# Optimization experiments

Hardware: AMD Instinct MI355X
Metric: run time of the kernel (lower is better)

Reference implementation:

```python
import jax, jax.numpy as jnp
import numpy as np

B, S, F_IN, E, H = 8, 1024, 512, 512, 8
C = E // H  # chunk size per head


def setup_inputs() -> dict:
    key = jax.random.key(0)
    ks = jax.random.split(key, 20)
    sF = 1.0 / np.sqrt(F_IN)
    sE = 1.0 / np.sqrt(E)
    d = {
        'x_real': jax.random.normal(ks[0], (B, S, F_IN), jnp.float32),
        'x_imag': jax.random.normal(ks[1], (B, S, F_IN), jnp.float32),
    }
    names = ['q', 'k', 'v']
    for i, n in enumerate(names):
        d[f'w{n}_r'] = jax.random.normal(ks[2 + 4 * i], (E, F_IN), jnp.float32) * sF
        d[f'w{n}_i'] = jax.random.normal(ks[3 + 4 * i], (E, F_IN), jnp.float32) * sF
        d[f'b{n}_r'] = jax.random.normal(ks[4 + 4 * i], (E,), jnp.float32) * sF
        d[f'b{n}_i'] = jax.random.normal(ks[5 + 4 * i], (E,), jnp.float32) * sF
    d['wo_r'] = jax.random.normal(ks[14], (F_IN, E), jnp.float32) * sE
    d['wo_i'] = jax.random.normal(ks[15], (F_IN, E), jnp.float32) * sE
    d['bo_r'] = jax.random.normal(ks[16], (F_IN,), jnp.float32) * sE
    d['bo_i'] = jax.random.normal(ks[17], (F_IN,), jnp.float32) * sE
    return d


def _cplx(r, i):
    return jax.lax.complex(r, i)


def _heads(y):
    # (B, S, E) -> (B, H, S, C); matches split(dim=2)+stack+transpose(0,1)
    return y.reshape(B, S, H, C).transpose(0, 2, 1, 3)


def reference(x_real, x_imag,
              wq_r, wq_i, bq_r, bq_i,
              wk_r, wk_i, bk_r, bk_i,
              wv_r, wv_i, bv_r, bv_i,
              wo_r, wo_i, bo_r, bo_i):
    x = _cplx(x_real, x_imag)
    wq, wk, wv = _cplx(wq_r, wq_i), _cplx(wk_r, wk_i), _cplx(wv_r, wv_i)
    bq, bk, bv = _cplx(bq_r, bq_i), _cplx(bk_r, bk_i), _cplx(bv_r, bv_i)
    wo, bo = _cplx(wo_r, wo_i), _cplx(bo_r, bo_i)

    q = _heads(jnp.einsum('bsf,ef->bse', x, wq) + bq)  # (B,H,S,C) complex
    k = _heads(jnp.einsum('bsf,ef->bse', x, wk) + bk)
    v = _heads(jnp.einsum('bsf,ef->bse', x, wv) + bv)

    divisor = jnp.sqrt(jnp.float32(2 * C))
    # Hermitian inner product: q @ conj(k)^T -> (B,H,S,S)
    sim = jnp.einsum('bhsc,bhtc->bhst', q, jnp.conj(k)) / divisor
    attn = jax.nn.softmax(jnp.abs(sim), axis=3).astype(jnp.complex64)
    # second Hermitian bmm: attn @ conj(v)
    av = jnp.einsum('bhst,bhtc->bhsc', attn, jnp.conj(v))
    concat = av.transpose(0, 2, 1, 3).reshape(B, S, E)
    out = jnp.einsum('bse,fe->bsf', concat, wo) + bo
    return out, attn
```

## Files before the change

kernel.cpp:

```cpp
#include <hip/hip_runtime.h>


namespace {
constexpr int Bn = 8, Sn = 1024, Fn = 512, En = 512, Hn = 8, Cn = 64;
constexpr int Mn = Bn * Sn;
constexpr int Qszi = Bn * Hn * Sn * Cn;
constexpr size_t Qsz = (size_t)Qszi;
constexpr int XLIM = Bn * Sn * Fn;
constexpr int WLIM = En * Fn;
constexpr size_t OUT1 = (size_t)Bn * Sn * Fn;
constexpr size_t ATT1 = (size_t)Bn * Hn * Sn * Sn;
constexpr float RDIV = 0.08838834764831845f;
}

typedef __attribute__((ext_vector_type(8))) short short8v;
typedef __attribute__((ext_vector_type(4))) float f32x4;

__device__ __forceinline__ size_t cmin(size_t i, size_t lim) { return i < lim ? i : lim; }

__device__ __forceinline__ float bf2f(unsigned short u) {
    union { unsigned int u32; float f; } c; c.u32 = (unsigned int)u << 16; return c.f;
}
__device__ __forceinline__ unsigned short f2bf(float f) {
    union { float f; unsigned int u; } c; c.f = f;
    unsigned int r = (c.u + 0x7FFFu + ((c.u >> 16) & 1u)) >> 16;
    return (unsigned short)r;
}
__device__ __forceinline__ unsigned int packbf(float lo, float hi) {
    return (unsigned int)f2bf(lo) | ((unsigned int)f2bf(hi) << 16);
}
__device__ __forceinline__ short8v neg8(short8v v) {
    union { short8v s; unsigned int u[4]; } c; c.s = v;
    #pragma unroll
    for (int j = 0; j < 4; ++j) c.u[j] ^= 0x80008000u;
    return c.s;
}

__device__ __forceinline__ float4 ld4(const float* p) { return *(const float4*)p; }
__device__ __forceinline__ float4 ld4(const unsigned short* p) {
    ushort4 v = *(const ushort4*)p;
    return make_float4(bf2f(v.x), bf2f(v.y), bf2f(v.z), bf2f(v.w));
}

template<bool CONJB>
__device__ __forceinline__ void mfma_body(
    const short (*As_r)[40], const short (*As_i)[40],
    const short (*Bs_r)[40], const short (*Bs_i)[40],
    int wr, int wn, int lrow, int lk,
    f32x4 accr[4][2], f32x4 acci[4][2])
{
    short8v a_r[4], a_i[4], a_x[4];
    #pragma unroll
    for (int fm = 0; fm < 4; ++fm) {
        a_r[fm] = *(const short8v*)&As_r[wr*64 + fm*16 + lrow][lk];
        a_i[fm] = *(const short8v*)&As_i[wr*64 + fm*16 + lrow][lk];
        a_x[fm] = neg8(CONJB ? a_r[fm] : a_i[fm]);
    }
    short8v b_r[2], b_i[2];
    #pragma unroll
    for (int fn = 0; fn < 2; ++fn) {
        b_r[fn] = *(const short8v*)&Bs_r[wn*32 + fn*16 + lrow][lk];
        b_i[fn] = *(const short8v*)&Bs_i[wn*32 + fn*16 + lrow][lk];
    }
    #pragma unroll
    for (int fm = 0; fm < 4; ++fm)
        #pragma unroll
        for (int fn = 0; fn < 2; ++fn) {
            accr[fm][fn] = __builtin_amdgcn_mfma_f32_16x16x32_bf16(
                a_r[fm], b_r[fn], accr[fm][fn], 0, 0, 0);
            accr[fm][fn] = __builtin_amdgcn_mfma_f32_16x16x32_bf16(
                CONJB ? a_i[fm] : a_x[fm], b_i[fn], accr[fm][fn], 0, 0, 0);
            acci[fm][fn] = __builtin_amdgcn_mfma_f32_16x16x32_bf16(
                CONJB ? a_x[fm] : a_r[fm], b_i[fn], acci[fm][fn], 0, 0, 0);
            acci[fm][fn] = __builtin_amdgcn_mfma_f32_16x16x32_bf16(
                a_i[fm], b_r[fn], acci[fm][fn], 0, 0, 0);
        }
}

template<bool CONJB>
__device__ __forceinline__ void cgemm_mfma(
    const float* __restrict__ Ar, const float* __restrict__ Ai, int arow0, int lda,
    const float* __restrict__ Br, const float* __restrict__ Bi, int brow0, int ldb,
    int K, f32x4 accr[4][2], f32x4 acci[4][2])
{
    __shared__ short As_r[128][40], As_i[128][40];
    __shared__ short Bs_r[64][40],  Bs_i[64][40];
    const int tid = threadIdx.x;
    const int sar = tid >> 1, sac = (tid & 1) * 16;
    const int sbr = tid >> 2, sbc = (tid & 3) * 8;
    const int wid = tid >> 6, lane = tid & 63;
    const int wr = wid >> 1, wn = wid & 1;
    const int lrow = lane & 15, lk = (lane >> 4) * 8;

    for (int k0 = 0; k0 < K; k0 += 32) {
        const float* pAr = Ar + (size_t)(arow0 + sar) * lda + k0 + sac;
        const float* pAi = Ai + (size_t)(arow0 + sar) * lda + k0 + sac;
        float4 va_r[4], va_i[4];
        #pragma unroll
        for (int q = 0; q < 4; ++q) { va_r[q] = ld4(pAr + 4*q); va_i[q] = ld4(pAi + 4*q); }
        const float* pBr = Br + (size_t)(brow0 + sbr) * ldb + k0 + sbc;
        const float* pBi = Bi + (size_t)(brow0 + sbr) * ldb + k0 + sbc;
        float4 vb_r[2], vb_i[2];
        #pragma unroll
        for (int q = 0; q < 2; ++q) { vb_r[q] = ld4(pBr + 4*q); vb_i[q] = ld4(pBi + 4*q); }

        __syncthreads();
        #pragma unroll
        for (int q = 0; q < 4; ++q) {
            *(uint2*)&As_r[sar][sac + 4*q] =
                make_uint2(packbf(va_r[q].x, va_r[q].y), packbf(va_r[q].z, va_r[q].w));
            *(uint2*)&As_i[sar][sac + 4*q] =
                make_uint2(packbf(va_i[q].x, va_i[q].y), packbf(va_i[q].z, va_i[q].w));
        }
        #pragma unroll
        for (int q = 0; q < 2; ++q) {
            *(uint2*)&Bs_r[sbr][sbc + 4*q] =
                make_uint2(packbf(vb_r[q].x, vb_r[q].y), packbf(vb_r[q].z, vb_r[q].w));
            *(uint2*)&Bs_i[sbr][sbc + 4*q] =
                make_uint2(packbf(vb_i[q].x, vb_i[q].y), packbf(vb_i[q].z, vb_i[q].w));
        }
        __syncthreads();
        mfma_body<CONJB>(As_r, As_i, Bs_r, Bs_i, wr, wn, lrow, lk, accr, acci);
    }
}

template<bool CONJB>
__device__ __forceinline__ void cgemm_mfma_bf16(
    const unsigned short* __restrict__ Ar, const unsigned short* __restrict__ Ai,
    int arow0, int lda,
    const unsigned short* __restrict__ Br, const unsigned short* __restrict__ Bi,
    int brow0, int ldb,
    int K, f32x4 accr[4][2], f32x4 acci[4][2])
{
    __shared__ short As_r[128][40], As_i[128][40];
    __shared__ short Bs_r[64][40],  Bs_i[64][40];
    const int tid = threadIdx.x;
    const int sar = tid >> 1, sac = (tid & 1) * 16;
    const int sbr = tid >> 2, sbc = (tid & 3) * 8;
    const int wid = tid >> 6, lane = tid & 63;
    const int wr = wid >> 1, wn = wid & 1;
    const int lrow = lane & 15, lk = (lane >> 4) * 8;

    for (int k0 = 0; k0 < K; k0 += 32) {
        const unsigned short* pAr = Ar + (size_t)(arow0 + sar) * lda + k0 + sac;
        const unsigned short* pAi = Ai + (size_t)(arow0 + sar) * lda + k0 + sac;
        short8v va_r0 = *(const short8v*)pAr;
        short8v va_r1 = *(const short8v*)(pAr + 8);
        short8v va_i0 = *(const short8v*)pAi;
        short8v va_i1 = *(const short8v*)(pAi + 8);
        const unsigned short* pBr = Br + (size_t)(brow0 + sbr) * ldb + k0 + sbc;
        const unsigned short* pBi = Bi + (size_t)(brow0 + sbr) * ldb + k0 + sbc;
        short8v vb_r = *(const short8v*)pBr;
        short8v vb_i = *(const short8v*)pBi;

        __syncthreads();
        *(short8v*)&As_r[sar][sac]     = va_r0;
        *(short8v*)&As_r[sar][sac + 8] = va_r1;
        *(short8v*)&As_i[sar][sac]     = va_i0;
        *(short8v*)&As_i[sar][sac + 8] = va_i1;
        *(short8v*)&Bs_r[sbr][sbc] = vb_r;
        *(short8v*)&Bs_i[sbr][sbc] = vb_i;
        __syncthreads();
        mfma_body<CONJB>(As_r, As_i, Bs_r, Bs_i, wr, wn, lrow, lk, accr, acci);
    }
}

__global__ void diag_k(float* __restrict__ out, float v) { out[0] = v; }

__global__ __launch_bounds__(256) void qkv_proj_k(
    const float* __restrict__ xr, const float* __restrict__ xi,
    const float* __restrict__ wqr, const float* __restrict__ wqi,
    const float* __restrict__ bqr, const float* __restrict__ bqi,
    const float* __restrict__ wkr, const float* __restrict__ wki,
    const float* __restrict__ bkr, const float* __restrict__ bki,
    const float* __restrict__ wvr, const float* __restrict__ wvi,
    const float* __restrict__ bvr, const float* __restrict__ bvi,
    unsigned short* __restrict__ ws)
{
    const int which = blockIdx.z;
    const float* wr_ = which == 0 ? wqr : which == 1 ? wkr : wvr;
    const float* wi_ = which == 0 ? wqi : which == 1 ? wki : wvi;
    const float* br_ = which == 0 ? bqr : which == 1 ? bkr : bvr;
    const float* bi_ = which == 0 ? bqi : which == 1 ? bki : bvi;
    unsigned short* outr = ws + (size_t)which * 2 * Qsz;
    unsigned short* outi = outr + Qsz;

    const int m0 = blockIdx.x * 128, n0 = blockIdx.y * 64;
    f32x4 accr[4][2], acci[4][2];
    const f32x4 z4 = {0.f, 0.f, 0.f, 0.f};
    #pragma unroll
    for (int fm = 0; fm < 4; ++fm)
        #pragma unroll
        for (int fn = 0; fn < 2; ++fn) { accr[fm][fn] = z4; acci[fm][fn] = z4; }

    cgemm_mfma<false>(xr, xi, m0, Fn, wr_, wi_, n0, Fn, Fn, accr, acci);

    const int lane = threadIdx.x & 63, wid = threadIdx.x >> 6;
    const int wr2 = wid >> 1, wn2 = wid & 1;
    #pragma unroll
    for (int fm = 0; fm < 4; ++fm)
        #pragma unroll
        for (int fn = 0; fn < 2; ++fn) {
            const int e = n0 + wn2*32 + fn*16 + (lane & 15);
            const int h = e >> 6, c = e & (Cn - 1);
            const float brv = br_[e], biv = bi_[e];
            #pragma unroll
            for (int r = 0; r < 4; ++r) {
                const int m = m0 + wr2*64 + fm*16 + (lane >> 4)*4 + r;
                const int b = m >> 10, s = m & (Sn - 1);
                const size_t idx = (((size_t)(b * Hn + h)) * Sn + s) * Cn + c;
                outr[idx] = f2bf(accr[fm][fn][r] + brv);
                outi[idx] = f2bf(acci[fm][fn][r] + biv);
            }
        }
}

template<int ST>
__global__ __launch_bounds__(256) void score_k(
    const unsigned short* __restrict__ qkv, float* __restrict__ attn)
{
    const int bh = blockIdx.z;
    const int r0 = blockIdx.x * 128, t0 = blockIdx.y * 64;
    const int row0 = bh * Sn;

    f32x4 accr[4][2], acci[4][2];
    const f32x4 z4 = {0.f, 0.f, 0.f, 0.f};
    #pragma unroll
    for (int fm = 0; fm < 4; ++fm)
        #pragma unroll
        for (int fn = 0; fn < 2; ++fn) { accr[fm][fn] = z4; acci[fm][fn] = z4; }

    cgemm_mfma_bf16<true>(qkv, qkv + Qsz, row0 + r0, Cn,
                          qkv + 2 * Qsz, qkv + 3 * Qsz, row0 + t0, Cn,
                          Cn, accr, acci);

    const size_t ATTF = ATT1 * ST;
    const int lane = threadIdx.x & 63, wid = threadIdx.x >> 6;
    const int wr2 = wid >> 1, wn2 = wid & 1;
    #pragma unroll
    for (int fm = 0; fm < 4; ++fm)
        #pragma unroll
        for (int fn = 0; fn < 2; ++fn) {
            const int t = t0 + wn2*32 + fn*16 + (lane & 15);
            #pragma unroll
            for (int r = 0; r < 4; ++r) {
                const int srow = r0 + wr2*64 + fm*16 + (lane >> 4)*4 + r;
                const size_t row = (size_t)bh * Sn + srow;
                const float re = accr[fm][fn][r], im = acci[fm][fn][r];
                const float mag = sqrtf(fmaf(re, re, im*im)) * RDIV;
                const size_t idx = cmin((row * Sn + t) * (size_t)ST, ATTF - ST);
                if (ST == 2) *(float2*)&attn[idx] = make_float2(mag, 0.f);
                else         attn[idx] = mag;
            }
        }
}

template<int ST>
__global__ __launch_bounds__(256) void softmax_k(float* __restrict__ attn)
{
    const int bh = blockIdx.y;
    const int wid = threadIdx.x >> 6, lane = threadIdx.x & 63;
    const int row = blockIdx.x * 4 + wid;
    const size_t rbase = ((size_t)bh * Sn + row) * Sn;
    const size_t ATTF = ATT1 * ST;

    float v[16];
    float mx = -1e30f;
    #pragma unroll
    for (int j = 0; j < 16; ++j) {
        v[j] = attn[cmin((rbase + lane + 64*j) * (size_t)ST, ATTF - ST)];
        mx = fmaxf(mx, v[j]);
    }
    #pragma unroll
    for (int m = 32; m >= 1; m >>= 1) mx = fmaxf(mx, __shfl_xor(mx, m));
    float sum = 0.f;
    #pragma unroll
    for (int j = 0; j < 16; ++j) { v[j] = __expf(v[j] - mx); sum += v[j]; }
    #pragma unroll
    for (int m = 32; m >= 1; m >>= 1) sum += __shfl_xor(sum, m);
    const float inv = 1.f / sum;
    #pragma unroll
    for (int j = 0; j < 16; ++j)
        attn[cmin((rbase + lane + 64*j) * (size_t)ST, ATTF - ST)] = v[j] * inv;
}

template<int ST>
__global__ __launch_bounds__(256) void av_k(
    const unsigned short* __restrict__ qkv, const float* __restrict__ attn,
    float* __restrict__ av)
{
    const int bh = blockIdx.y;
    const int r0 = blockIdx.x * 128;
    const size_t voff = (size_t)bh * Sn * Cn;
    const unsigned short* vr = qkv + 4 * Qsz + voff;
    const unsigned short* vi = qkv + 5 * Qsz + voff;
    const size_t abase = ((size_t)bh * Sn + r0) * Sn;

    __shared__ short Ps[128][40];
    __shared__ short Vtr[64][40], Vti[64][40];

    const int tid = threadIdx.x;
    const int spr = tid >> 1, spt = (tid & 1) * 16;
    const int svt = tid & 31, svc = (tid >> 5) * 8;
    const int wid = tid >> 6, lane = tid & 63;
    const int wr = wid >> 1, wn = wid & 1;
    const int lrow = lane & 15, lk = (lane >> 4) * 8;

    f32x4 accr[4][2], acci[4][2];
    const f32x4 z4 = {0.f, 0.f, 0.f, 0.f};
    #pragma unroll
    for (int fm = 0; fm < 4; ++fm)
        #pragma unroll
        for (int fn = 0; fn < 2; ++fn) { accr[fm][fn] = z4; acci[fm][fn] = z4; }

    for (int t0 = 0; t0 < Sn; t0 += 32) {
        float pv[16];
        if (ST == 2) {
            const float4* ap4 = (const float4*)((const float2*)attn +
                                 (abase + (size_t)spr * Sn + t0 + spt));
            #pragma unroll
            for (int q = 0; q < 8; ++q) { float4 v4 = ap4[q]; pv[2*q] = v4.x; pv[2*q+1] = v4.z; }
        } else {
            const float* ap = attn + abase + (size_t)spr * Sn + t0 + spt;
            #pragma unroll
            for (int q = 0; q < 4; ++q) {
                float4 v4 = *(const float4*)(ap + 4*q);
                pv[4*q] = v4.x; pv[4*q+1] = v4.y; pv[4*q+2] = v4.z; pv[4*q+3] = v4.w;
            }
        }
        short8v vvr = *(const short8v*)(vr + (size_t)(t0 + svt) * Cn + svc);
        short8v vvi = *(const short8v*)(vi + (size_t)(t0 + svt) * Cn + svc);

        __syncthreads();
        #pragma unroll
        for (int q = 0; q < 4; ++q)
            *(unsigned int*)&Ps[spr][spt + 4*q] =
                (unsigned int)f2bf(pv[4*q])     | ((unsigned int)f2bf(pv[4*q+1]) << 16),
            *(unsigned int*)&Ps[spr][spt + 4*q + 2] =
                (unsigned int)f2bf(pv[4*q+2])   | ((unsigned int)f2bf(pv[4*q+3]) << 16);
        #pragma unroll
        for (int j = 0; j < 8; ++j) {
            Vtr[svc + j][svt] = vvr[j];
            Vti[svc + j][svt] = vvi[j];
        }
        __syncthreads();

        short8v pA[4];
        #pragma unroll
        for (int fm = 0; fm < 4; ++fm)
            pA[fm] = *(const short8v*)&Ps[wr*64 + fm*16 + lrow][lk];
        short8v bR[2], bI[2];
        #pragma unroll
        for (int fn = 0; fn < 2; ++fn) {
            bR[fn] = *(const short8v*)&Vtr[wn*32 + fn*16 + lrow][lk];
            bI[fn] = *(const short8v*)&Vti[wn*32 + fn*16 + lrow][lk];
        }
        #pragma unroll
        for (int fm = 0; fm < 4; ++fm)
            #pragma unroll
            for (int fn = 0; fn < 2; ++fn) {
                accr[fm][fn] = __builtin_amdgcn_mfma_f32_16x16x32_bf16(
                    pA[fm], bR[fn], accr[fm][fn], 0, 0, 0);
                acci[fm][fn] = __builtin_amdgcn_mfma_f32_16x16x32_bf16(
                    pA[fm], bI[fn], acci[fm][fn], 0, 0, 0);
            }
    }

    const int b = bh >> 3, h = bh & 7;
    #pragma unroll
    for (int fm = 0; fm < 4; ++fm)
        #pragma unroll
        for (int fn = 0; fn < 2; ++fn) {
            const int c = wn*32 + fn*16 + (lane & 15);
            #pragma unroll
            for (int r = 0; r < 4; ++r) {
                const int srow = r0 + wr*64 + fm*16 + (lane >> 4)*4 + r;
                const size_t base = ((size_t)(b * Sn + srow)) * En + h * Cn + c;
                av[base]       =  accr[fm][fn][r];
                av[Qsz + base] = -acci[fm][fn][r];
            }
        }
}

template<int ST>
__global__ __launch_bounds__(256) void out_proj_k(
    const float* __restrict__ avr, const float* __restrict__ avi,
    const float* __restrict__ wor, const float* __restrict__ woi,
    const float* __restrict__ bor, const float* __restrict__ boi,
    float* __restrict__ out)
{
    const int m0 = blockIdx.x * 128, n0 = blockIdx.y * 64;
    f32x4 accr[4][2], acci[4][2];
    const f32x4 z4 = {0.f, 0.f, 0.f, 0.f};
    #pragma unroll
    for (int fm = 0; fm < 4; ++fm)
        #pragma unroll
        for (int fn = 0; fn < 2; ++fn) { accr[fm][fn] = z4; acci[fm][fn] = z4; }

    cgemm_mfma<false>(avr, avi, m0, En, wor, woi, n0, En, En, accr, acci);

    const int lane = threadIdx.x & 63, wid = threadIdx.x >> 6;
    const int wr2 = wid >> 1, wn2 = wid & 1;
    #pragma unroll
    for (int fm = 0; fm < 4; ++fm)
        #pragma unroll
        for (int fn = 0; fn < 2; ++fn) {
            const int f = n0 + wn2*32 + fn*16 + (lane & 15);
            const float brv = bor[f], biv = boi[f];
            #pragma unroll
            for (int r = 0; r < 4; ++r) {
                const int m = m0 + wr2*64 + fm*16 + (lane >> 4)*4 + r;
                const size_t idx = ((size_t)m * Fn + f) * (size_t)ST;
                if (ST == 2)
                    *(float2*)&out[idx] = make_float2(accr[fm][fn][r] + brv, acci[fm][fn][r] + biv);
                else
                    out[idx] = accr[fm][fn][r] + brv;
            }
        }
}

template<int ST>
static void launch_all(const float* xr, const float* xi,
                       const float* wqr, const float* wqi, const float* bqr, const float* bqi,
                       const float* wkr, const float* wki, const float* bkr, const float* bki,
                       const float* wvr, const float* wvi, const float* bvr, const float* bvi,
                       const float* wor, const float* woi, const float* bor, const float* boi,
                       unsigned short* qkv, float* av, float* out, hipStream_t stream)
{
    float* attn = out + OUT1 * ST;
    qkv_proj_k<<<dim3(Mn/128, En/64, 3), 256, 0, stream>>>(
        xr, xi, wqr, wqi, bqr, bqi, wkr, wki, bkr, bki, wvr, wvi, bvr, bvi, qkv);
    score_k<ST><<<dim3(Sn/128, Sn/64, Bn*Hn), 256, 0, stream>>>(qkv, attn);
    softmax_k<ST><<<dim3(Sn/4, Bn*Hn), 256, 0, stream>>>(attn);
    av_k<ST><<<dim3(Sn/128, Bn*Hn), 256, 0, stream>>>(qkv, attn, av);
    out_proj_k<ST><<<dim3(Mn/128, Fn/64), 256, 0, stream>>>(
        av, av + Qsz, wor, woi, bor, boi, out);
}

extern "C" void kernel_launch(void* const* d_in, const int* in_sizes, int n_in,
                              void* d_out, int out_size, void* d_ws, size_t ws_size,
                              hipStream_t stream)
{
    bool sizes_ok = (n_in == 18);
    if (sizes_ok) {
        sizes_ok = in_sizes[0] == XLIM && in_sizes[1] == XLIM;
        for (int g = 0; g < 3 && sizes_ok; ++g) {
            sizes_ok = in_sizes[2 + 4*g] == WLIM && in_sizes[3 + 4*g] == WLIM &&
                       in_sizes[4 + 4*g] == En  && in_sizes[5 + 4*g] == En;
        }
        sizes_ok = sizes_ok && in_sizes[14] == WLIM && in_sizes[15] == WLIM &&
                   in_sizes[16] == Fn && in_sizes[17] == Fn;
    }
    const size_t ws_needed = 6 * Qsz * sizeof(unsigned short);
    const bool ws_ok = (d_ws != nullptr) && (ws_size >= ws_needed);

    const long long fullF = 2LL * (long long)(OUT1 + ATT1);
    const long long realF = (long long)(OUT1 + ATT1);
    const int st = ((long long)out_size == fullF) ? 2
                 : ((long long)out_size == realF) ? 1 : 0;

    if (!sizes_ok || !ws_ok || st == 0) {
        float diag = !sizes_ok ? 3.0e9f
                   : !ws_ok    ? (float)(double)ws_size
                               : (float)out_size;
        diag_k<<<1, 1, 0, stream>>>((float*)d_out, diag);
        return;
    }

    const float* xr  = (const float*)d_in[0];
    const float* xi  = (const float*)d_in[1];
    const float* wqr = (const float*)d_in[2];
    const float* wqi = (const float*)d_in[3];
    const float* bqr = (const float*)d_in[4];
    const float* bqi = (const float*)d_in[5];
    const float* wkr = (const float*)d_in[6];
    const float* wki = (const float*)d_in[7];
    const float* bkr = (const float*)d_in[8];
    const float* bki = (const float*)d_in[9];
    const float* wvr = (const float*)d_in[10];
    const float* wvi = (const float*)d_in[11];
    const float* bvr = (const float*)d_in[12];
    const float* bvi = (const float*)d_in[13];
    const float* wor = (const float*)d_in[14];
    const float* woi = (const float*)d_in[15];
    const float* bor = (const float*)d_in[16];
    const float* boi = (const float*)d_in[17];

    unsigned short* qkv = (unsigned short*)d_ws;
    float* av = (float*)d_ws;
    float* out = (float*)d_out;

    if (st == 2)
        launch_all<2>(xr, xi, wqr, wqi, bqr, bqi, wkr, wki, bkr, bki,
                      wvr, wvi, bvr, bvi, wor, woi, bor, boi, qkv, av, out, stream);
    else
        launch_all<1>(xr, xi, wqr, wqi, bqr, bqi, wkr, wki, bkr, bki,
                      wvr, wvi, bvr, bvi, wor, woi, bor, boi, qkv, av, out, stream);
}
```

Before: 394.5 us.

## Fuse score, softmax and attn@V into one two-pass attention kernel

Replaces the separate score, softmax and attn@V kernels with one kernel per (batch-head, 128-row) tile. A first pass recomputes the Hermitian QK scores to build softmax row sums. A second pass recomputes them, writes normalized probabilities once, and multiplies them by V from LDS. Since |sim| is non-negative and small, the row max is skipped. This removes the read-modify-write round trips of the large attention matrix through global memory, at the cost of computing QK twice. The attention-value output is now stored as bf16 in a separate workspace region, which halves the out-projection A-operand traffic and requires a larger workspace.

```diff
diff --git a/kernel.cpp b/kernel.cpp
--- a/kernel.cpp
+++ b/kernel.cpp
@@ -16,8 +16,6 @@
 typedef __attribute__((ext_vector_type(8))) short short8v;
 typedef __attribute__((ext_vector_type(4))) float f32x4;
 
-__device__ __forceinline__ size_t cmin(size_t i, size_t lim) { return i < lim ? i : lim; }
-
 __device__ __forceinline__ float bf2f(unsigned short u) {
     union { unsigned int u32; float f; } c; c.u32 = (unsigned int)u << 16; return c.f;
 }
@@ -35,12 +33,7 @@
     for (int j = 0; j < 4; ++j) c.u[j] ^= 0x80008000u;
     return c.s;
 }
-
 __device__ __forceinline__ float4 ld4(const float* p) { return *(const float4*)p; }
-__device__ __forceinline__ float4 ld4(const unsigned short* p) {
-    ushort4 v = *(const ushort4*)p;
-    return make_float4(bf2f(v.x), bf2f(v.y), bf2f(v.z), bf2f(v.w));
-}
 
 template<bool CONJB>
 __device__ __forceinline__ void mfma_body(
@@ -125,11 +118,10 @@
 }
 
 template<bool CONJB>
-__device__ __forceinline__ void cgemm_mfma_bf16(
+__device__ __forceinline__ void cgemm_mfma_abf16(
     const unsigned short* __restrict__ Ar, const unsigned short* __restrict__ Ai,
     int arow0, int lda,
-    const unsigned short* __restrict__ Br, const unsigned short* __restrict__ Bi,
-    int brow0, int ldb,
+    const float* __restrict__ Br, const float* __restrict__ Bi, int brow0, int ldb,
     int K, f32x4 accr[4][2], f32x4 acci[4][2])
 {
     __shared__ short As_r[128][40], As_i[128][40];
@@ -148,18 +140,24 @@
         short8v va_r1 = *(const short8v*)(pAr + 8);
         short8v va_i0 = *(const short8v*)pAi;
         short8v va_i1 = *(const short8v*)(pAi + 8);
-        const unsigned short* pBr = Br + (size_t)(brow0 + sbr) * ldb + k0 + sbc;
-        const unsigned short* pBi = Bi + (size_t)(brow0 + sbr) * ldb + k0 + sbc;
-        short8v vb_r = *(const short8v*)pBr;
-        short8v vb_i = *(const short8v*)pBi;
+        const float* pBr = Br + (size_t)(brow0 + sbr) * ldb + k0 + sbc;
+        const float* pBi = Bi + (size_t)(brow0 + sbr) * ldb + k0 + sbc;
+        float4 vb_r[2], vb_i[2];
+        #pragma unroll
+        for (int q = 0; q < 2; ++q) { vb_r[q] = ld4(pBr + 4*q); vb_i[q] = ld4(pBi + 4*q); }
 
         __syncthreads();
         *(short8v*)&As_r[sar][sac]     = va_r0;
         *(short8v*)&As_r[sar][sac + 8] = va_r1;
         *(short8v*)&As_i[sar][sac]     = va_i0;
         *(short8v*)&As_i[sar][sac + 8] = va_i1;
-        *(short8v*)&Bs_r[sbr][sbc] = vb_r;
-        *(short8v*)&Bs_i[sbr][sbc] = vb_i;
+        #pragma unroll
+        for (int q = 0; q < 2; ++q) {
+            *(uint2*)&Bs_r[sbr][sbc + 4*q] =
+                make_uint2(packbf(vb_r[q].x, vb_r[q].y), packbf(vb_r[q].z, vb_r[q].w));
+            *(uint2*)&Bs_i[sbr][sbc + 4*q] =
+                make_uint2(packbf(vb_i[q].x, vb_i[q].y), packbf(vb_i[q].z, vb_i[q].w));
+        }
         __syncthreads();
         mfma_body<CONJB>(As_r, As_i, Bs_r, Bs_i, wr, wn, lrow, lk, accr, acci);
     }
@@ -216,175 +214,237 @@
 }
 
 template<int ST>
-__global__ __launch_bounds__(256) void score_k(
-    const unsigned short* __restrict__ qkv, float* __restrict__ attn)
-{
-    const int bh = blockIdx.z;
-    const int r0 = blockIdx.x * 128, t0 = blockIdx.y * 64;
-    const int row0 = bh * Sn;
-
-    f32x4 accr[4][2], acci[4][2];
-    const f32x4 z4 = {0.f, 0.f, 0.f, 0.f};
-    #pragma unroll
-    for (int fm = 0; fm < 4; ++fm)
-        #pragma unroll
-        for (int fn = 0; fn < 2; ++fn) { accr[fm][fn] = z4; acci[fm][fn] = z4; }
-
-    cgemm_mfma_bf16<true>(qkv, qkv + Qsz, row0 + r0, Cn,
-                          qkv + 2 * Qsz, qkv + 3 * Qsz, row0 + t0, Cn,
-                          Cn, accr, acci);
-
-    const size_t ATTF = ATT1 * ST;
-    const int lane = threadIdx.x & 63, wid = threadIdx.x >> 6;
-    const int wr2 = wid >> 1, wn2 = wid & 1;
-    #pragma unroll
-    for (int fm = 0; fm < 4; ++fm)
-        #pragma unroll
-        for (int fn = 0; fn < 2; ++fn) {
-            const int t = t0 + wn2*32 + fn*16 + (lane & 15);
-            #pragma unroll
-            for (int r = 0; r < 4; ++r) {
-                const int srow = r0 + wr2*64 + fm*16 + (lane >> 4)*4 + r;
-                const size_t row = (size_t)bh * Sn + srow;
-                const float re = accr[fm][fn][r], im = acci[fm][fn][r];
-                const float mag = sqrtf(fmaf(re, re, im*im)) * RDIV;
-                const size_t idx = cmin((row * Sn + t) * (size_t)ST, ATTF - ST);
-                if (ST == 2) *(float2*)&attn[idx] = make_float2(mag, 0.f);
-                else         attn[idx] = mag;
-            }
-        }
-}
-
-template<int ST>
-__global__ __launch_bounds__(256) void softmax_k(float* __restrict__ attn)
-{
-    const int bh = blockIdx.y;
-    const int wid = threadIdx.x >> 6, lane = threadIdx.x & 63;
-    const int row = blockIdx.x * 4 + wid;
-    const size_t rbase = ((size_t)bh * Sn + row) * Sn;
-    const size_t ATTF = ATT1 * ST;
-
-    float v[16];
-    float mx = -1e30f;
-    #pragma unroll
-    for (int j = 0; j < 16; ++j) {
-        v[j] = attn[cmin((rbase + lane + 64*j) * (size_t)ST, ATTF - ST)];
-        mx = fmaxf(mx, v[j]);
-    }
-    #pragma unroll
-    for (int m = 32; m >= 1; m >>= 1) mx = fmaxf(mx, __shfl_xor(mx, m));
-    float sum = 0.f;
-    #pragma unroll
-    for (int j = 0; j < 16; ++j) { v[j] = __expf(v[j] - mx); sum += v[j]; }
-    #pragma unroll
-    for (int m = 32; m >= 1; m >>= 1) sum += __shfl_xor(sum, m);
-    const float inv = 1.f / sum;
-    #pragma unroll
-    for (int j = 0; j < 16; ++j)
-        attn[cmin((rbase + lane + 64*j) * (size_t)ST, ATTF - ST)] = v[j] * inv;
-}
-
-template<int ST>
-__global__ __launch_bounds__(256) void av_k(
-    const unsigned short* __restrict__ qkv, const float* __restrict__ attn,
-    float* __restrict__ av)
+__global__ __launch_bounds__(256) void attn_fused_k(
+    const unsigned short* __restrict__ qkv, float* __restrict__ attn,
+    unsigned short* __restrict__ avb)
 {
     const int bh = blockIdx.y;
     const int r0 = blockIdx.x * 128;
-    const size_t voff = (size_t)bh * Sn * Cn;
-    const unsigned short* vr = qkv + 4 * Qsz + voff;
-    const unsigned short* vi = qkv + 5 * Qsz + voff;
-    const size_t abase = ((size_t)bh * Sn + r0) * Sn;
-
-    __shared__ short Ps[128][40];
-    __shared__ short Vtr[64][40], Vti[64][40];
+    const size_t poff = (size_t)bh * Sn * Cn;
+    const unsigned short* qr = qkv + poff;
+    const unsigned short* qi = qkv + Qsz + poff;
+    const unsigned short* kr = qkv + 2 * Qsz + poff;
+    const unsigned short* ki = qkv + 3 * Qsz + poff;
+    const unsigned short* vr = qkv + 4 * Qsz + poff;
+    const unsigned short* vi = qkv + 5 * Qsz + poff;
+
+    __shared__ short Qr[128][68], Qi[128][68];
+    __shared__ short KP[2][64][68];
+    __shared__ short Vtr[64][68], Vti[64][68];
+    short (*Ps)[68] = (short(*)[68])KP;
 
     const int tid = threadIdx.x;
-    const int spr = tid >> 1, spt = (tid & 1) * 16;
-    const int svt = tid & 31, svc = (tid >> 5) * 8;
-    const int wid = tid >> 6, lane = tid & 63;
+    const int lane = tid & 63, wid = tid >> 6;
+    const int lrow = lane & 15, g = lane >> 4, lk = g * 8;
+    const int srow0 = 32 * wid;
     const int wr = wid >> 1, wn = wid & 1;
-    const int lrow = lane & 15, lk = (lane >> 4) * 8;
-
-    f32x4 accr[4][2], acci[4][2];
+
+    {
+        const int row = tid >> 1, seg = (tid & 1) * 32;
+        const unsigned short* pr = qr + (size_t)(r0 + row) * Cn + seg;
+        const unsigned short* pi = qi + (size_t)(r0 + row) * Cn + seg;
+        #pragma unroll
+        for (int q = 0; q < 4; ++q) {
+            *(short8v*)&Qr[row][seg + 8*q] = *(const short8v*)(pr + 8*q);
+            *(short8v*)&Qi[row][seg + 8*q] = *(const short8v*)(pi + 8*q);
+        }
+    }
+    const int kst_row = tid >> 2, kst_seg = (tid & 3) * 16;
+    const int vst_t = tid & 63, vst_c = (tid >> 6) * 16;
+
+    float ssum[2][4] = {};
+    __syncthreads();
+
+    for (int t0 = 0; t0 < Sn; t0 += 64) {
+        short8v k_r0 = *(const short8v*)(kr + (size_t)(t0 + kst_row) * Cn + kst_seg);
+        short8v k_r1 = *(const short8v*)(kr + (size_t)(t0 + kst_row) * Cn + kst_seg + 8);
+        short8v k_i0 = *(const short8v*)(ki + (size_t)(t0 + kst_row) * Cn + kst_seg);
+        short8v k_i1 = *(const short8v*)(ki + (size_t)(t0 + kst_row) * Cn + kst_seg + 8);
+        __syncthreads();
+        *(short8v*)&KP[0][kst_row][kst_seg]     = k_r0;
+        *(short8v*)&KP[0][kst_row][kst_seg + 8] = k_r1;
+        *(short8v*)&KP[1][kst_row][kst_seg]     = k_i0;
+        *(short8v*)&KP[1][kst_row][kst_seg + 8] = k_i1;
+        __syncthreads();
+
+        f32x4 cr[2][4], ci[2][4];
+        const f32x4 z4 = {0.f, 0.f, 0.f, 0.f};
+        #pragma unroll
+        for (int fm = 0; fm < 2; ++fm)
+            #pragma unroll
+            for (int fn = 0; fn < 4; ++fn) { cr[fm][fn] = z4; ci[fm][fn] = z4; }
+        #pragma unroll
+        for (int kh = 0; kh < 2; ++kh) {
+            const int kof = kh*32 + lk;
+            short8v br_[4], bi_[4];
+            #pragma unroll
+            for (int fn = 0; fn < 4; ++fn) {
+                br_[fn] = *(const short8v*)&KP[0][fn*16 + lrow][kof];
+                bi_[fn] = *(const short8v*)&KP[1][fn*16 + lrow][kof];
+            }
+            #pragma unroll
+            for (int fm = 0; fm < 2; ++fm) {
+                short8v ar = *(const short8v*)&Qr[srow0 + fm*16 + lrow][kof];
+                short8v ai = *(const short8v*)&Qi[srow0 + fm*16 + lrow][kof];
+                short8v ax = neg8(ar);
+                #pragma unroll
+                for (int fn = 0; fn < 4; ++fn) {
+                    cr[fm][fn] = __builtin_amdgcn_mfma_f32_16x16x32_bf16(ar, br_[fn], cr[fm][fn], 0,0,0);
+                    cr[fm][fn] = __builtin_amdgcn_mfma_f32_16x16x32_bf16(ai, bi_[fn], cr[fm][fn], 0,0,0);
+                    ci[fm][fn] = __builtin_amdgcn_mfma_f32_16x16x32_bf16(ai, br_[fn], ci[fm][fn], 0,0,0);
+                    ci[fm][fn] = __builtin_amdgcn_mfma_f32_16x16x32_bf16(ax, bi_[fn], ci[fm][fn], 0,0,0);
+                }
+            }
+        }
+        #pragma unroll
+        for (int fm = 0; fm < 2; ++fm)
+            #pragma unroll
+            for (int rr = 0; rr < 4; ++rr) {
+                float acc = 0.f;
+                #pragma unroll
+                for (int fn = 0; fn < 4; ++fn) {
+                    const float re = cr[fm][fn][rr], im = ci[fm][fn][rr];
+                    acc += __expf(sqrtf(fmaf(re, re, im*im)) * RDIV);
+                }
+                ssum[fm][rr] += acc;
+            }
+    }
+    float inv[2][4];
+    #pragma unroll
+    for (int fm = 0; fm < 2; ++fm)
+        #pragma unroll
+        for (int rr = 0; rr < 4; ++rr) {
+            float s = ssum[fm][rr];
+            s += __shfl_xor(s, 1); s += __shfl_xor(s, 2);
+            s += __shfl_xor(s, 4); s += __shfl_xor(s, 8);
+            inv[fm][rr] = 1.f / s;
+        }
+
+    f32x4 pvr[4][2], pvi[4][2];
     const f32x4 z4 = {0.f, 0.f, 0.f, 0.f};
     #pragma unroll
     for (int fm = 0; fm < 4; ++fm)
         #pragma unroll
-        for (int fn = 0; fn < 2; ++fn) { accr[fm][fn] = z4; acci[fm][fn] = z4; }
-
-    for (int t0 = 0; t0 < Sn; t0 += 32) {
-        float pv[16];
-        if (ST == 2) {
-            const float4* ap4 = (const float4*)((const float2*)attn +
-                                 (abase + (size_t)spr * Sn + t0 + spt));
-            #pragma unroll
-            for (int q = 0; q < 8; ++q) { float4 v4 = ap4[q]; pv[2*q] = v4.x; pv[2*q+1] = v4.z; }
-        } else {
-            const float* ap = attn + abase + (size_t)spr * Sn + t0 + spt;
-            #pragma unroll
-            for (int q = 0; q < 4; ++q) {
-                float4 v4 = *(const float4*)(ap + 4*q);
-                pv[4*q] = v4.x; pv[4*q+1] = v4.y; pv[4*q+2] = v4.z; pv[4*q+3] = v4.w;
-            }
-        }
-        short8v vvr = *(const short8v*)(vr + (size_t)(t0 + svt) * Cn + svc);
-        short8v vvi = *(const short8v*)(vi + (size_t)(t0 + svt) * Cn + svc);
-
-        __syncthreads();
-        #pragma unroll
-        for (int q = 0; q < 4; ++q)
-            *(unsigned int*)&Ps[spr][spt + 4*q] =
-                (unsigned int)f2bf(pv[4*q])     | ((unsigned int)f2bf(pv[4*q+1]) << 16),
-            *(unsigned int*)&Ps[spr][spt + 4*q + 2] =
-                (unsigned int)f2bf(pv[4*q+2])   | ((unsigned int)f2bf(pv[4*q+3]) << 16);
+        for (int fn = 0; fn < 2; ++fn) { pvr[fm][fn] = z4; pvi[fm][fn] = z4; }
+
+    for (int t0 = 0; t0 < Sn; t0 += 64) {
+        short8v k_r0 = *(const short8v*)(kr + (size_t)(t0 + kst_row) * Cn + kst_seg);
+        short8v k_r1 = *(const short8v*)(kr + (size_t)(t0 + kst_row) * Cn + kst_seg + 8);
+        short8v k_i0 = *(const short8v*)(ki + (size_t)(t0 + kst_row) * Cn + kst_seg);
+        short8v k_i1 = *(const short8v*)(ki + (size_t)(t0 + kst_row) * Cn + kst_seg + 8);
+        short8v v_r0 = *(const short8v*)(vr + (size_t)(t0 + vst_t) * Cn + vst_c);
+        short8v v_r1 = *(const short8v*)(vr + (size_t)(t0 + vst_t) * Cn + vst_c + 8);
+        short8v v_i0 = *(const short8v*)(vi + (size_t)(t0 + vst_t) * Cn + vst_c);
+        short8v v_i1 = *(const short8v*)(vi + (size_t)(t0 + vst_t) * Cn + vst_c + 8);
+        __syncthreads();
+        *(short8v*)&KP[0][kst_row][kst_seg]     = k_r0;
+        *(short8v*)&KP[0][kst_row][kst_seg + 8] = k_r1;
+        *(short8v*)&KP[1][kst_row][kst_seg]     = k_i0;
+        *(short8v*)&KP[1][kst_row][kst_seg + 8] = k_i1;
         #pragma unroll
         for (int j = 0; j < 8; ++j) {
-            Vtr[svc + j][svt] = vvr[j];
-            Vti[svc + j][svt] = vvi[j];
-        }
-        __syncthreads();
-
-        short8v pA[4];
-        #pragma unroll
-        for (int fm = 0; fm < 4; ++fm)
-            pA[fm] = *(const short8v*)&Ps[wr*64 + fm*16 + lrow][lk];
-        short8v bR[2], bI[2];
+            Vtr[vst_c + j][vst_t] = v_r0[j];
+            Vtr[vst_c + 8 + j][vst_t] = v_r1[j];
+            Vti[vst_c + j][vst_t] = v_i0[j];
+            Vti[vst_c + 8 + j][vst_t] = v_i1[j];
+        }
+        __syncthreads();
+
+        f32x4 cr[2][4], ci[2][4];
+        #pragma unroll
+        for (int fm = 0; fm < 2; ++fm)
+            #pragma unroll
+            for (int fn = 0; fn < 4; ++fn) { cr[fm][fn] = z4; ci[fm][fn] = z4; }
+        #pragma unroll
+        for (int kh = 0; kh < 2; ++kh) {
+            const int kof = kh*32 + lk;
+            short8v br_[4], bi_[4];
+            #pragma unroll
+            for (int fn = 0; fn < 4; ++fn) {
+                br_[fn] = *(const short8v*)&KP[0][fn*16 + lrow][kof];
+                bi_[fn] = *(const short8v*)&KP[1][fn*16 + lrow][kof];
+            }
+            #pragma unroll
+            for (int fm = 0; fm < 2; ++fm) {
+                short8v ar = *(const short8v*)&Qr[srow0 + fm*16 + lrow][kof];
+                short8v ai = *(const short8v*)&Qi[srow0 + fm*16 + lrow][kof];
+                short8v ax = neg8(ar);
+                #pragma unroll
+                for (int fn = 0; fn < 4; ++fn) {
+                    cr[fm][fn] = __builtin_amdgcn_mfma_f32_16x16x32_bf16(ar, br_[fn], cr[fm][fn], 0,0,0);
+                    cr[fm][fn] = __builtin_amdgcn_mfma_f32_16x16x32_bf16(ai, bi_[fn], cr[fm][fn], 0,0,0);
+                    ci[fm][fn] = __builtin_amdgcn_mfma_f32_16x16x32_bf16(ai, br_[fn], ci[fm][fn], 0,0,0);
+                    ci[fm][fn] = __builtin_amdgcn_mfma_f32_16x16x32_bf16(ax, bi_[fn], ci[fm][fn], 0,0,0);
+                }
+            }
+        }
+        float pval[2][4][4];
+        #pragma unroll
+        for (int fm = 0; fm < 2; ++fm)
+            #pragma unroll
+            for (int fn = 0; fn < 4; ++fn) {
+                const int t = t0 + fn*16 + lrow;
+                #pragma unroll
+                for (int rr = 0; rr < 4; ++rr) {
+                    const float re = cr[fm][fn][rr], im = ci[fm][fn][rr];
+                    const float p = __expf(sqrtf(fmaf(re, re, im*im)) * RDIV) * inv[fm][rr];
+                    pval[fm][fn][rr] = p;
+                    const size_t row = (size_t)bh * Sn + r0 + srow0 + fm*16 + g*4 + rr;
+                    const size_t idx = (row * Sn + t) * (size_t)ST;
+                    if (ST == 2) *(float2*)&attn[idx] = make_float2(p, 0.f);
+                    else         attn[idx] = p;
+                }
+            }
+        __syncthreads();
+        #pragma unroll
+        for (int fm = 0; fm < 2; ++fm)
+            #pragma unroll
+            for (int fn = 0; fn < 4; ++fn)
+                #pragma unroll
+                for (int rr = 0; rr < 4; ++rr)
+                    Ps[srow0 + fm*16 + g*4 + rr][fn*16 + lrow] = f2bf(pval[fm][fn][rr]);
+        __syncthreads();
+
+        #pragma unroll
+        for (int kh = 0; kh < 2; ++kh) {
+            const int kof = kh*32 + lk;
+            short8v bR[2], bI[2];
+            #pragma unroll
+            for (int fn = 0; fn < 2; ++fn) {
+                bR[fn] = *(const short8v*)&Vtr[wn*32 + fn*16 + lrow][kof];
+                bI[fn] = *(const short8v*)&Vti[wn*32 + fn*16 + lrow][kof];
+            }
+            #pragma unroll
+            for (int fm = 0; fm < 4; ++fm) {
+                short8v pA = *(const short8v*)&Ps[wr*64 + fm*16 + lrow][kof];
+                #pragma unroll
+                for (int fn = 0; fn < 2; ++fn) {
+                    pvr[fm][fn] = __builtin_amdgcn_mfma_f32_16x16x32_bf16(pA, bR[fn], pvr[fm][fn], 0,0,0);
+                    pvi[fm][fn] = __builtin_amdgcn_mfma_f32_16x16x32_bf16(pA, bI[fn], pvi[fm][fn], 0,0,0);
+                }
+            }
+        }
+    }
+
+    const int b = bh >> 3, h = bh & 7;
+    #pragma unroll
+    for (int fm = 0; fm < 4; ++fm)
         #pragma unroll
         for (int fn = 0; fn < 2; ++fn) {
-            bR[fn] = *(const short8v*)&Vtr[wn*32 + fn*16 + lrow][lk];
-            bI[fn] = *(const short8v*)&Vti[wn*32 + fn*16 + lrow][lk];
-        }
-        #pragma unroll
-        for (int fm = 0; fm < 4; ++fm)
-            #pragma unroll
-            for (int fn = 0; fn < 2; ++fn) {
-                accr[fm][fn] = __builtin_amdgcn_mfma_f32_16x16x32_bf16(
-                    pA[fm], bR[fn], accr[fm][fn], 0, 0, 0);
-                acci[fm][fn] = __builtin_amdgcn_mfma_f32_16x16x32_bf16(
-                    pA[fm], bI[fn], acci[fm][fn], 0, 0, 0);
-            }
-    }
-
-    const int b = bh >> 3, h = bh & 7;
-    #pragma unroll
-    for (int fm = 0; fm < 4; ++fm)
-        #pragma unroll
-        for (int fn = 0; fn < 2; ++fn) {
-            const int c = wn*32 + fn*16 + (lane & 15);
-            #pragma unroll
-            for (int r = 0; r < 4; ++r) {
-                const int srow = r0 + wr*64 + fm*16 + (lane >> 4)*4 + r;
-                const size_t base = ((size_t)(b * Sn + srow)) * En + h * Cn + c;
-                av[base]       =  accr[fm][fn][r];
-                av[Qsz + base] = -acci[fm][fn][r];
+            const int c = wn*32 + fn*16 + lrow;
+            #pragma unroll
+            for (int rr = 0; rr < 4; ++rr) {
+                const int row = r0 + wr*64 + fm*16 + g*4 + rr;
+                const size_t addr = ((size_t)(b * Sn + row)) * En + h * Cn + c;
+                avb[addr]       = f2bf( pvr[fm][fn][rr]);
+                avb[Qsz + addr] = f2bf(-pvi[fm][fn][rr]);
             }
         }
 }
 
 template<int ST>
 __global__ __launch_bounds__(256) void out_proj_k(
-    const float* __restrict__ avr, const float* __restrict__ avi,
+    const unsigned short* __restrict__ avr, const unsigned short* __restrict__ avi,
     const float* __restrict__ wor, const float* __restrict__ woi,
     const float* __restrict__ bor, const float* __restrict__ boi,
     float* __restrict__ out)
@@ -397,7 +457,7 @@
         #pragma unroll
         for (int fn = 0; fn < 2; ++fn) { accr[fm][fn] = z4; acci[fm][fn] = z4; }
 
-    cgemm_mfma<false>(avr, avi, m0, En, wor, woi, n0, En, En, accr, acci);
+    cgemm_mfma_abf16<false>(avr, avi, m0, En, wor, woi, n0, En, En, accr, acci);
 
     const int lane = threadIdx.x & 63, wid = threadIdx.x >> 6;
     const int wr2 = wid >> 1, wn2 = wid & 1;
@@ -425,16 +485,14 @@
                        const float* wkr, const float* wki, const float* bkr, const float* bki,
                        const float* wvr, const float* wvi, const float* bvr, const float* bvi,
                        const float* wor, const float* woi, const float* bor, const float* boi,
-                       unsigned short* qkv, float* av, float* out, hipStream_t stream)
+                       unsigned short* qkv, unsigned short* avb, float* out, hipStream_t stream)
 {
     float* attn = out + OUT1 * ST;
     qkv_proj_k<<<dim3(Mn/128, En/64, 3), 256, 0, stream>>>(
         xr, xi, wqr, wqi, bqr, bqi, wkr, wki, bkr, bki, wvr, wvi, bvr, bvi, qkv);
-    score_k<ST><<<dim3(Sn/128, Sn/64, Bn*Hn), 256, 0, stream>>>(qkv, attn);
-    softmax_k<ST><<<dim3(Sn/4, Bn*Hn), 256, 0, stream>>>(attn);
-    av_k<ST><<<dim3(Sn/128, Bn*Hn), 256, 0, stream>>>(qkv, attn, av);
+    attn_fused_k<ST><<<dim3(Sn/128, Bn*Hn), 256, 0, stream>>>(qkv, attn, avb);
     out_proj_k<ST><<<dim3(Mn/128, Fn/64), 256, 0, stream>>>(
-        av, av + Qsz, wor, woi, bor, boi, out);
+        avb, avb + Qsz, wor, woi, bor, boi, out);
 }
 
 extern "C" void kernel_launch(void* const* d_in, const int* in_sizes, int n_in,
@@ -451,7 +509,7 @@
         sizes_ok = sizes_ok && in_sizes[14] == WLIM && in_sizes[15] == WLIM &&
                    in_sizes[16] == Fn && in_sizes[17] == Fn;
     }
-    const size_t ws_needed = 6 * Qsz * sizeof(unsigned short);
+    const size_t ws_needed = 8 * Qsz * sizeof(unsigned short);
     const bool ws_ok = (d_ws != nullptr) && (ws_size >= ws_needed);
 
     const long long fullF = 2LL * (long long)(OUT1 + ATT1);
@@ -487,13 +545,13 @@
     const float* boi = (const float*)d_in[17];
 
     unsigned short* qkv = (unsigned short*)d_ws;
-    float* av = (float*)d_ws;
+    unsigned short* avb = qkv + 6 * Qsz;
     float* out = (float*)d_out;
 
     if (st == 2)
         launch_all<2>(xr, xi, wqr, wqi, bqr, bqi, wkr, wki, bkr, bki,
-                      wvr, wvi, bvr, bvi, wor, woi, bor, boi, qkv, av, out, stream);
+                      wvr, wvi, bvr, bvi, wor, woi, bor, boi, qkv, avb, out, stream);
     else
         launch_all<1>(xr, xi, wqr, wqi, bqr, bqi, wkr, wki, bkr, bki,
-                      wvr, wvi, bvr, bvi, wor, woi, bor, boi, qkv, av, out, stream);
-}
+                      wvr, wvi, bvr, bvi, wor, woi, bor, boi, qkv, avb, out, stream);
+}
```

Measured after the change: 316.8 us (median of 2 runs). 1.25x faster.
